# Kernel optimization log

Hardware: AMD Instinct MI355X
Metric: run time of the kernel (lower is better)

## Reference

```python
import jax, jax.numpy as jnp
from jax import lax
import numpy as np

TWO_PI = 2.0 * np.pi

# ---- batched real-amplitude statevector simulator (RY/CNOT only -> real state) ----

def _init_state(batch, n):
    s = jnp.zeros((batch, 2 ** n), dtype=jnp.float32).at[:, 0].set(1.0)
    return s.reshape((batch,) + (2,) * n)

def _ry(state, wire, theta, n):
    # state: (B, 2,...,2); theta: scalar or (B,)
    ax = wire + 1
    h = theta * 0.5
    c = jnp.reshape(jnp.cos(h), (-1,) + (1,) * (n - 1))
    s = jnp.reshape(jnp.sin(h), (-1,) + (1,) * (n - 1))
    s0 = lax.index_in_dim(state, 0, ax, keepdims=False)
    s1 = lax.index_in_dim(state, 1, ax, keepdims=False)
    return jnp.stack([c * s0 - s * s1, s * s0 + c * s1], axis=ax)

def _cnot(state, ctrl, tgt):
    axc, axt = ctrl + 1, tgt + 1
    s0 = lax.index_in_dim(state, 0, axc, keepdims=True)
    s1 = lax.index_in_dim(state, 1, axc, keepdims=True)
    return jnp.concatenate([s0, jnp.flip(s1, axis=axt)], axis=axc)

def _expz(state, wire, n):
    sgn = jnp.reshape(jnp.array([1.0, -1.0], state.dtype),
                      (1,) * (wire + 1) + (2,) + (1,) * (n - wire - 1))
    return jnp.sum(state * state * sgn, axis=tuple(range(1, n + 1)))

# gate lists: ('ry', theta_index, wire) or ('cx', control, target)
EDGE_OPS = [('ry',0,0),('ry',1,1),('cx',0,1),('ry',2,2),('ry',3,3),('cx',3,2),
            ('ry',4,4),('ry',5,5),('cx',4,5),('ry',6,6),('ry',7,7),('cx',7,6),
            ('ry',8,1),('ry',9,2),('cx',1,2),('ry',10,5),('ry',11,6),('cx',6,5),
            ('ry',12,2),('ry',13,5),('cx',2,5),('ry',14,5)]

NODE_OPS = [('ry',0,0),('ry',1,1),('cx',0,1),('ry',2,2),('ry',3,3),('cx',3,2),
            ('ry',4,4),('ry',5,5),('cx',4,5),('ry',6,6),('ry',7,7),('cx',7,6),
            ('ry',8,8),('ry',9,9),('cx',8,9),('ry',10,10),('ry',11,11),('cx',11,10),
            ('ry',12,1),('ry',13,2),('cx',1,2),('ry',14,5),('ry',15,6),('cx',6,5),
            ('ry',16,9),('ry',17,10),('cx',10,9),('ry',18,2),('ry',19,5),('cx',2,5),
            ('ry',20,5),('ry',21,9),('cx',5,9),('ry',22,4)]

def _circuit(angles, theta, ops, n, meas_wire):
    st = _init_state(angles.shape[0], n)
    for i in range(n):  # input encoding RYs, per-sample angles
        st = _ry(st, i, angles[:, i], n)
    for op in ops:
        if op[0] == 'ry':
            st = _ry(st, op[2], theta[op[1]], n)
        else:
            st = _cnot(st, op[1], op[2])
    return _expz(st, meas_wire, n)

# ---- GNN pieces ----

def _edge_net(H, Ri, Ro, theta):
    bo = Ro.T @ H                      # [E,4]
    bi = Ri.T @ H                      # [E,4]
    B = jnp.concatenate([bo, bi], axis=1)  # [E,8]
    return (1.0 - _circuit(B, theta, EDGE_OPS, 8, 5)) * 0.5

def _node_net(H, e, Ri, Ro, theta):
    bo = Ro.T @ H                      # [E,4]
    bi = Ri.T @ H                      # [E,4]
    mi = (Ri * e[None, :]) @ bo        # [N,4]
    mo = (Ro * e[None, :]) @ bi        # [N,4]
    M = jnp.concatenate([mi, mo, H], axis=1)  # [N,12]
    return jnp.pi * (1.0 - _circuit(M, theta, NODE_OPS, 12, 9))

def _gnn(X, Ri, Ro, W_in, b_in, theta_edge, theta_node, n_iters=2):
    H = jnp.concatenate([jax.nn.sigmoid(X @ W_in + b_in) * TWO_PI, X], axis=1)  # [N,4]
    e = _edge_net(H, Ri, Ro, theta_edge)
    for _ in range(n_iters):
        h = _node_net(H, e, Ri, Ro, theta_node)   # [N]
        H = jnp.concatenate([h[:, None], X], axis=1)
        e = _edge_net(H, Ri, Ro, theta_edge)
    return e


def setup_inputs() -> dict:
    key = jax.random.key(0)
    ks = jax.random.split(key, 6)
    N, E = 2048, 4096
    X = jax.random.normal(ks[0], (N, 3), jnp.float32)
    recv = jax.random.randint(ks[1], (E,), 0, N)
    send = jax.random.randint(ks[2], (E,), 0, N)
    cols = jnp.arange(E)
    Ri = jnp.zeros((N, E), jnp.float32).at[recv, cols].set(1.0)
    Ro = jnp.zeros((N, E), jnp.float32).at[send, cols].set(1.0)
    W_in = jax.random.normal(ks[3], (3, 1), jnp.float32)
    b_in = jnp.zeros((1,), jnp.float32)
    theta_edge = jax.random.uniform(ks[4], (15,), jnp.float32, 0.0, TWO_PI)
    theta_node = jax.random.uniform(ks[5], (23,), jnp.float32, 0.0, TWO_PI)
    return {'X': X, 'Ri': Ri, 'Ro': Ro, 'W_in': W_in, 'b_in': b_in,
            'theta_edge': theta_edge, 'theta_node': theta_node}


def reference(X, Ri, Ro, W_in, b_in, theta_edge, theta_node):
    return _gnn(X, Ri, Ro, W_in, b_in, theta_edge, theta_node, n_iters=2)
```

## Files before the change

kernel.cpp:

```cpp
#include <hip/hip_runtime.h>
#include <math.h>

#define N_NODES 2048
#define N_EDGES 4096
#define PI_F 3.14159265358979323846f
#define TWO_PI_F 6.28318530717958647692f

#define NBLK 256
#define NTHR 256
#define NSCAN (NBLK * NTHR)
#define TOT4 (N_NODES * N_EDGES / 4)

__device__ __forceinline__ float agent_load(const float* p) {
    return __hip_atomic_load(p, __ATOMIC_RELAXED, __HIP_MEMORY_SCOPE_AGENT);
}
__device__ __forceinline__ int agent_load_i(const int* p) {
    return __hip_atomic_load(p, __ATOMIC_RELAXED, __HIP_MEMORY_SCOPE_AGENT);
}
__device__ __forceinline__ void agent_store(float* p, float v) {
    __hip_atomic_store(p, v, __ATOMIC_RELAXED, __HIP_MEMORY_SCOPE_AGENT);
}
__device__ __forceinline__ void agent_store_i(int* p, int v) {
    __hip_atomic_store(p, v, __ATOMIC_RELAXED, __HIP_MEMORY_SCOPE_AGENT);
}
__device__ __forceinline__ void spin_ge(const int* p, int v) {
    while (__hip_atomic_load(p, __ATOMIC_RELAXED, __HIP_MEMORY_SCOPE_AGENT) < v)
        __builtin_amdgcn_s_sleep(2);
    asm volatile("" ::: "memory");
}


template<int M>
__device__ __forceinline__ void ry16(float* a, float c, float s) {
#pragma unroll
    for (int i = 0; i < 16; ++i)
        if (!(i & M)) {
            int j = i | M;
            float x0 = a[i], x1 = a[j];
            a[i] = c * x0 - s * x1;
            a[j] = s * x0 + c * x1;
        }
}
template<int MC, int MT>
__device__ __forceinline__ void cx16(float* a) {
#pragma unroll
    for (int i = 0; i < 16; ++i)
        if ((i & MC) && !(i & MT)) {
            int j = i | MT;
            float t = a[i]; a[i] = a[j]; a[j] = t;
        }
}

template<bool BTYPE>
__device__ __forceinline__ void sub16(const float* ic, const float* is,
                                      const float* thc, const float* ths,
                                      float& z, float& x) {
    float a[16];
    a[0] = ic[3]; a[1] = is[3];
#pragma unroll
    for (int i = 0; i < 2; ++i) { a[i | 2] = a[i] * is[2]; a[i] *= ic[2]; }
#pragma unroll
    for (int i = 0; i < 4; ++i) { a[i | 4] = a[i] * is[1]; a[i] *= ic[1]; }
#pragma unroll
    for (int i = 0; i < 8; ++i) { a[i | 8] = a[i] * is[0]; a[i] *= ic[0]; }
    ry16<8>(a, thc[0], ths[0]);
    ry16<4>(a, thc[1], ths[1]);
    cx16<8, 4>(a);
    ry16<2>(a, thc[2], ths[2]);
    ry16<1>(a, thc[3], ths[3]);
    cx16<1, 2>(a);
    ry16<4>(a, thc[4], ths[4]);
    ry16<2>(a, thc[5], ths[5]);
    if (BTYPE) { cx16<2, 4>(a); ry16<4>(a, thc[6], ths[6]); }
    else       { cx16<4, 2>(a); ry16<2>(a, thc[6], ths[6]); }
    const int m = BTYPE ? 4 : 2;
    z = 0.f; x = 0.f;
#pragma unroll
    for (int i = 0; i < 16; ++i) z += (i & m) ? -a[i] * a[i] : a[i] * a[i];
    if (BTYPE) {
#pragma unroll
        for (int i = 0; i < 16; ++i) if (!(i & 4)) x += a[i] * a[i | 4];
        x *= 2.f;
    }
}

__device__ __forceinline__ void edge_pub(
        float chh, float shh, const float* cxv, const float* sxv,
        const float* teC, const float* teS,
        float& zA, float& zB, float& xB) {
    float ic[4] = {chh, cxv[0], cxv[1], cxv[2]};
    float is[4] = {shh, sxv[0], sxv[1], sxv[2]};
    float dmy;
    {
        float thc[7] = {teC[0], teC[1], teC[2], teC[3], teC[8], teC[9], teC[12]};
        float ths[7] = {teS[0], teS[1], teS[2], teS[3], teS[8], teS[9], teS[12]};
        sub16<false>(ic, is, thc, ths, zA, dmy);
    }
    {
        float thc[7] = {teC[4], teC[5], teC[6], teC[7], teC[10], teC[11], teC[13]};
        float ths[7] = {teS[4], teS[5], teS[6], teS[7], teS[10], teS[11], teS[13]};
        sub16<true>(ic, is, thc, ths, zB, xB);
    }
}

__device__ __forceinline__ void scatter8(float ev, const float4& Hs, const float4& Hr,
                                         int si, int ri,
                                         float* __restrict__ macc, int* __restrict__ arr) {
    atomicAdd(&macc[ri*8+0], ev*Hs.x); atomicAdd(&macc[ri*8+1], ev*Hs.y);
    atomicAdd(&macc[ri*8+2], ev*Hs.z); atomicAdd(&macc[ri*8+3], ev*Hs.w);
    atomicAdd(&macc[si*8+4], ev*Hr.x); atomicAdd(&macc[si*8+5], ev*Hr.y);
    atomicAdd(&macc[si*8+6], ev*Hr.z); atomicAdd(&macc[si*8+7], ev*Hr.w);
    asm volatile("s_waitcnt vmcnt(0)" ::: "memory");
    atomicAdd(&arr[ri], 1); atomicAdd(&arr[si], 1);
}

__global__ __launch_bounds__(256) void k_fused(
        const float* __restrict__ X, const float* __restrict__ Ri,
        const float* __restrict__ Ro, const float* __restrict__ W,
        const float* __restrict__ b, const float* __restrict__ te,
        const float* __restrict__ tn,
        float* __restrict__ H, float* __restrict__ pub,
        int* __restrict__ send, int* __restrict__ recv,
        float* __restrict__ maccA, float* __restrict__ maccB,
        int* __restrict__ arrA, int* __restrict__ arrB,
        int* __restrict__ epoch, int* __restrict__ deg,
        int* __restrict__ sdone, float* __restrict__ out) {
    int blk = blockIdx.x, tid = threadIdx.x;
    bool edge_actor = (blk < 64)              && (tid < 64);
    bool node_actor = (blk >= 64 && blk < 96) && (tid < 64);

    float chh = 0.f, shh = 0.f, cxv[3], sxv[3];
    float teC[14], teS[14], tnC[22], tnS[22];
    float C14 = 0.f, S14 = 0.f;

    if (edge_actor) {
        float c, s;
        __sincosf(0.5f * te[14], &s, &c);
        C14 = c*c - s*s;
        S14 = 2.f*c*s;
    }
    if (node_actor) {
        int n = (blk - 64) * 64 + tid;
        float x0 = X[n*3+0], x1 = X[n*3+1], x2 = X[n*3+2];
        float z = x0*W[0] + x1*W[1] + x2*W[2] + b[0];
        float sg = 1.0f / (1.0f + __expf(-z));
        float h = sg * TWO_PI_F;
        __sincosf(0.5f*h,  &shh, &chh);
        __sincosf(0.5f*x0, &sxv[0], &cxv[0]);
        __sincosf(0.5f*x1, &sxv[1], &cxv[1]);
        __sincosf(0.5f*x2, &sxv[2], &cxv[2]);
#pragma unroll
        for (int k = 0; k < 14; ++k) __sincosf(0.5f*te[k], &teS[k], &teC[k]);
#pragma unroll
        for (int k = 0; k < 22; ++k) __sincosf(0.5f*tn[k], &tnS[k], &tnC[k]);
        float zA, zB, xB;
        edge_pub(chh, shh, cxv, sxv, teC, teS, zA, zB, xB);
        agent_store(&pub[n*4+0], zA);
        agent_store(&pub[n*4+1], zB);
        agent_store(&pub[n*4+2], xB);
        agent_store(&H[n*4+0], h);
        agent_store(&H[n*4+1], x0);
        agent_store(&H[n*4+2], x1);
        agent_store(&H[n*4+3], x2);
    }

    {
        int gid = blk * NTHR + tid;
        const float4* Ri4 = (const float4*)Ri;
        const float4* Ro4 = (const float4*)Ro;
#pragma unroll 1
        for (int t0 = gid; t0 < TOT4; t0 += 4 * NSCAN) {
            float4 vi[4], vo[4];
#pragma unroll
            for (int u = 0; u < 4; ++u) {
                int t = t0 + u * NSCAN;
                vi[u] = Ri4[t]; vo[u] = Ro4[t];
            }
#pragma unroll
            for (int u = 0; u < 4; ++u) {
                int t = t0 + u * NSCAN;
                int base = t * 4;
                int row = base >> 12;
                int e   = base & (N_EDGES - 1);
                int cnt = 0;
                if (vi[u].x != 0.f) { agent_store_i(recv+e+0, row); ++cnt; }
                if (vi[u].y != 0.f) { agent_store_i(recv+e+1, row); ++cnt; }
                if (vi[u].z != 0.f) { agent_store_i(recv+e+2, row); ++cnt; }
                if (vi[u].w != 0.f) { agent_store_i(recv+e+3, row); ++cnt; }
                if (vo[u].x != 0.f) { agent_store_i(send+e+0, row); ++cnt; }
                if (vo[u].y != 0.f) { agent_store_i(send+e+1, row); ++cnt; }
                if (vo[u].z != 0.f) { agent_store_i(send+e+2, row); ++cnt; }
                if (vo[u].w != 0.f) { agent_store_i(send+e+3, row); ++cnt; }
                if (cnt) atomicAdd(&deg[row], cnt);
            }
        }
        asm volatile("s_waitcnt vmcnt(0)" ::: "memory");
        __syncthreads();
        if (tid == 0) atomicAdd(sdone, 1);
    }

    if (!edge_actor && !node_actor) return;
    int lane = tid;

    spin_ge(sdone, NBLK);

    if (edge_actor) {
        int e = blk * 64 + lane;
        int si = agent_load_i(send + e);
        int ri = agent_load_i(recv + e);
        float4 Hs, Hr;
        Hs.x = agent_load(H+si*4+0); Hs.y = agent_load(H+si*4+1);
        Hs.z = agent_load(H+si*4+2); Hs.w = agent_load(H+si*4+3);
        Hr.x = agent_load(H+ri*4+0); Hr.y = agent_load(H+ri*4+1);
        Hr.z = agent_load(H+ri*4+2); Hr.w = agent_load(H+ri*4+3);

        float zA = agent_load(&pub[si*4+0]);
        float zB = agent_load(&pub[ri*4+1]);
        float xB = agent_load(&pub[ri*4+2]);
        float ev = 0.5f*(1.f - (C14*zA*zB - S14*xB));
        scatter8(ev, Hs, Hr, si, ri, maccA, arrA);

        spin_ge(epoch + si, 1); spin_ge(epoch + ri, 1);
        zA = agent_load(&pub[si*4+0]);
        zB = agent_load(&pub[ri*4+1]);
        xB = agent_load(&pub[ri*4+2]);
        Hs.x = agent_load(&H[si*4]);
        Hr.x = agent_load(&H[ri*4]);
        ev = 0.5f*(1.f - (C14*zA*zB - S14*xB));
        scatter8(ev, Hs, Hr, si, ri, maccB, arrB);

        spin_ge(epoch + si, 2); spin_ge(epoch + ri, 2);
        zA = agent_load(&pub[si*4+0]);
        zB = agent_load(&pub[ri*4+1]);
        xB = agent_load(&pub[ri*4+2]);
        out[e] = 0.5f*(1.f - (C14*zA*zB - S14*xB));
        return;
    }

    int n = (blk - 64) * 64 + lane;
    int dg = agent_load_i(deg + n);
    float C20 = tnC[20]*tnC[20] - tnS[20]*tnS[20];
    float S20 = 2.f*tnC[20]*tnS[20];

    for (int it = 0; it < 2; ++it) {
        const float* mc_ = it ? maccB : maccA;
        const int*   ar  = it ? arrB  : arrA;
        float zB9, dmy;
        {
            float ic[4] = {chh, cxv[0], cxv[1], cxv[2]};
            float is[4] = {shh, sxv[0], sxv[1], sxv[2]};
            float thc[7] = {tnC[8],tnC[9],tnC[10],tnC[11],tnC[16],tnC[17],tnC[21]};
            float ths[7] = {tnS[8],tnS[9],tnS[10],tnS[11],tnS[16],tnS[17],tnS[21]};
            sub16<true>(ic, is, thc, ths, zB9, dmy);
        }
        spin_ge(ar + n, dg);
        float M[8], mC[8], mS[8];
#pragma unroll
        for (int k = 0; k < 8; ++k) M[k] = agent_load(mc_ + n*8 + k);
#pragma unroll
        for (int k = 0; k < 8; ++k) __sincosf(0.5f*M[k], &mS[k], &mC[k]);
        float zA1, zA2, xA2;
        {
            float thc[7] = {tnC[0],tnC[1],tnC[2],tnC[3],tnC[12],tnC[13],tnC[18]};
            float ths[7] = {tnS[0],tnS[1],tnS[2],tnS[3],tnS[12],tnS[13],tnS[18]};
            sub16<false>(&mC[0], &mS[0], thc, ths, zA1, dmy);
        }
        {
            float thc[7] = {tnC[4],tnC[5],tnC[6],tnC[7],tnC[14],tnC[15],tnC[19]};
            float ths[7] = {tnS[4],tnS[5],tnS[6],tnS[7],tnS[14],tnS[15],tnS[19]};
            sub16<true>(&mC[4], &mS[4], thc, ths, zA2, xA2);
        }
        float p9 = (C20*zA1*zA2 - S20*xA2) * zB9;
        float h = PI_F * (1.f - p9);
        __sincosf(0.5f*h, &shh, &chh);
        float zAe, zBe, xBe;
        edge_pub(chh, shh, cxv, sxv, teC, teS, zAe, zBe, xBe);
        agent_store(&pub[n*4+0], zAe);
        agent_store(&pub[n*4+1], zBe);
        agent_store(&pub[n*4+2], xBe);
        agent_store(&H[n*4], h);
        asm volatile("s_waitcnt vmcnt(0)" ::: "memory");
        agent_store_i(epoch + n, it + 1);
    }
}

extern "C" void kernel_launch(void* const* d_in, const int* in_sizes, int n_in,
                              void* d_out, int out_size, void* d_ws, size_t ws_size,
                              hipStream_t stream) {
    const float* X  = (const float*)d_in[0];
    const float* Ri = (const float*)d_in[1];
    const float* Ro = (const float*)d_in[2];
    const float* W  = (const float*)d_in[3];
    const float* b  = (const float*)d_in[4];
    const float* te = (const float*)d_in[5];
    const float* tn = (const float*)d_in[6];
    float* out = (float*)d_out;

    float* H     = (float*)d_ws;
    float* pub   = H + N_NODES * 4;
    int*   send  = (int*)(pub + N_NODES * 4);
    int*   recv  = send + N_EDGES;
    float* maccA = (float*)(recv + N_EDGES);
    float* maccB = maccA + N_NODES * 8;
    int*   arrA  = (int*)(maccB + N_NODES * 8);
    int*   arrB  = arrA + N_NODES;
    int*   epoch = arrB + N_NODES;
    int*   deg   = epoch + N_NODES;
    int*   sdone = deg + N_NODES;
    size_t zbytes = (size_t)(2*N_NODES*8 + 4*N_NODES + 16) * 4;

    hipMemsetAsync((void*)maccA, 0, zbytes, stream);
    k_fused<<<NBLK, NTHR, 0, stream>>>(X, Ri, Ro, W, b, te, tn,
                                       H, pub, send, recv,
                                       maccA, maccB, arrA, arrB,
                                       epoch, deg, sdone, out);
}
```

Baseline: 129.0 us.

## Drop node-actor blocks; edges recompute endpoint node states redundantly

Removes the separate node-actor blocks and the epoch/pub handshake. Each edge thread now recomputes the node-state updates for its sender and receiver directly from the accumulated messages. Edge threads wait per-edge on the send/recv index (stored +1 so zero means not yet written) instead of on the global scan-done barrier, and theta sincos values are shared through LDS. The scan is also unrolled 8 deep instead of 4. This removes a cross-block dependency chain in exchange for duplicated node computation per edge and a larger memset.

```diff
diff --git a/kernel.cpp b/kernel.cpp
--- a/kernel.cpp
+++ b/kernel.cpp
@@ -16,9 +16,6 @@
 }
 __device__ __forceinline__ int agent_load_i(const int* p) {
     return __hip_atomic_load(p, __ATOMIC_RELAXED, __HIP_MEMORY_SCOPE_AGENT);
-}
-__device__ __forceinline__ void agent_store(float* p, float v) {
-    __hip_atomic_store(p, v, __ATOMIC_RELAXED, __HIP_MEMORY_SCOPE_AGENT);
 }
 __device__ __forceinline__ void agent_store_i(int* p, int v) {
     __hip_atomic_store(p, v, __ATOMIC_RELAXED, __HIP_MEMORY_SCOPE_AGENT);
@@ -84,23 +81,36 @@
     }
 }
 
-__device__ __forceinline__ void edge_pub(
-        float chh, float shh, const float* cxv, const float* sxv,
-        const float* teC, const float* teS,
-        float& zA, float& zB, float& xB) {
-    float ic[4] = {chh, cxv[0], cxv[1], cxv[2]};
-    float is[4] = {shh, sxv[0], sxv[1], sxv[2]};
-    float dmy;
-    {
-        float thc[7] = {teC[0], teC[1], teC[2], teC[3], teC[8], teC[9], teC[12]};
-        float ths[7] = {teS[0], teS[1], teS[2], teS[3], teS[8], teS[9], teS[12]};
-        sub16<false>(ic, is, thc, ths, zA, dmy);
-    }
-    {
-        float thc[7] = {teC[4], teC[5], teC[6], teC[7], teC[10], teC[11], teC[13]};
-        float ths[7] = {teS[4], teS[5], teS[6], teS[7], teS[10], teS[11], teS[13]};
-        sub16<true>(ic, is, thc, ths, zB, xB);
-    }
+__device__ __forceinline__ float node_update(
+        const float* M, float& chh, float& shh,
+        const float* cxv, const float* sxv,
+        const float* tnC, const float* tnS, float C20, float S20) {
+    float zB9, dmy;
+    {
+        float ic[4] = {chh, cxv[0], cxv[1], cxv[2]};
+        float is[4] = {shh, sxv[0], sxv[1], sxv[2]};
+        float thc[7] = {tnC[8],tnC[9],tnC[10],tnC[11],tnC[16],tnC[17],tnC[21]};
+        float ths[7] = {tnS[8],tnS[9],tnS[10],tnS[11],tnS[16],tnS[17],tnS[21]};
+        sub16<true>(ic, is, thc, ths, zB9, dmy);
+    }
+    float mC[8], mS[8];
+#pragma unroll
+    for (int k = 0; k < 8; ++k) __sincosf(0.5f * M[k], &mS[k], &mC[k]);
+    float zA1, zA2, xA2;
+    {
+        float thc[7] = {tnC[0],tnC[1],tnC[2],tnC[3],tnC[12],tnC[13],tnC[18]};
+        float ths[7] = {tnS[0],tnS[1],tnS[2],tnS[3],tnS[12],tnS[13],tnS[18]};
+        sub16<false>(&mC[0], &mS[0], thc, ths, zA1, dmy);
+    }
+    {
+        float thc[7] = {tnC[4],tnC[5],tnC[6],tnC[7],tnC[14],tnC[15],tnC[19]};
+        float ths[7] = {tnS[4],tnS[5],tnS[6],tnS[7],tnS[14],tnS[15],tnS[19]};
+        sub16<true>(&mC[4], &mS[4], thc, ths, zA2, xA2);
+    }
+    float p9 = (C20*zA1*zA2 - S20*xA2) * zB9;
+    float h = PI_F * (1.f - p9);
+    __sincosf(0.5f*h, &shh, &chh);
+    return h;
 }
 
 __device__ __forceinline__ void scatter8(float ev, const float4& Hs, const float4& Hr,
@@ -119,49 +129,28 @@
         const float* __restrict__ Ro, const float* __restrict__ W,
         const float* __restrict__ b, const float* __restrict__ te,
         const float* __restrict__ tn,
-        float* __restrict__ H, float* __restrict__ pub,
         int* __restrict__ send, int* __restrict__ recv,
         float* __restrict__ maccA, float* __restrict__ maccB,
         int* __restrict__ arrA, int* __restrict__ arrB,
-        int* __restrict__ epoch, int* __restrict__ deg,
-        int* __restrict__ sdone, float* __restrict__ out) {
+        int* __restrict__ deg, int* __restrict__ sdone,
+        float* __restrict__ out) {
+    __shared__ float s_teC[16], s_teS[16], s_tnC[24], s_tnS[24];
     int blk = blockIdx.x, tid = threadIdx.x;
-    bool edge_actor = (blk < 64)              && (tid < 64);
-    bool node_actor = (blk >= 64 && blk < 96) && (tid < 64);
-
-    float chh = 0.f, shh = 0.f, cxv[3], sxv[3];
-    float teC[14], teS[14], tnC[22], tnS[22];
-    float C14 = 0.f, S14 = 0.f;
-
-    if (edge_actor) {
-        float c, s;
-        __sincosf(0.5f * te[14], &s, &c);
-        C14 = c*c - s*s;
-        S14 = 2.f*c*s;
-    }
-    if (node_actor) {
-        int n = (blk - 64) * 64 + tid;
-        float x0 = X[n*3+0], x1 = X[n*3+1], x2 = X[n*3+2];
-        float z = x0*W[0] + x1*W[1] + x2*W[2] + b[0];
-        float sg = 1.0f / (1.0f + __expf(-z));
-        float h = sg * TWO_PI_F;
-        __sincosf(0.5f*h,  &shh, &chh);
-        __sincosf(0.5f*x0, &sxv[0], &cxv[0]);
-        __sincosf(0.5f*x1, &sxv[1], &cxv[1]);
-        __sincosf(0.5f*x2, &sxv[2], &cxv[2]);
-#pragma unroll
-        for (int k = 0; k < 14; ++k) __sincosf(0.5f*te[k], &teS[k], &teC[k]);
-#pragma unroll
-        for (int k = 0; k < 22; ++k) __sincosf(0.5f*tn[k], &tnS[k], &tnC[k]);
-        float zA, zB, xB;
-        edge_pub(chh, shh, cxv, sxv, teC, teS, zA, zB, xB);
-        agent_store(&pub[n*4+0], zA);
-        agent_store(&pub[n*4+1], zB);
-        agent_store(&pub[n*4+2], xB);
-        agent_store(&H[n*4+0], h);
-        agent_store(&H[n*4+1], x0);
-        agent_store(&H[n*4+2], x1);
-        agent_store(&H[n*4+3], x2);
+    bool edge_blk = (blk < 64);
+
+    if (edge_blk) {
+        if (tid < 14) {
+            float s, c; __sincosf(0.5f * te[tid], &s, &c);
+            s_teC[tid] = c; s_teS[tid] = s;
+        } else if (tid == 14) {
+            float s, c; __sincosf(te[14], &s, &c);
+            s_teC[14] = c; s_teS[14] = s;
+        } else if (tid < 15 + 22) {
+            int k = tid - 15; float s, c;
+            if (k == 20) __sincosf(tn[20], &s, &c);
+            else         __sincosf(0.5f * tn[k], &s, &c);
+            s_tnC[k] = c; s_tnS[k] = s;
+        }
     }
 
     {
@@ -169,28 +158,28 @@
         const float4* Ri4 = (const float4*)Ri;
         const float4* Ro4 = (const float4*)Ro;
 #pragma unroll 1
-        for (int t0 = gid; t0 < TOT4; t0 += 4 * NSCAN) {
-            float4 vi[4], vo[4];
-#pragma unroll
-            for (int u = 0; u < 4; ++u) {
+        for (int t0 = gid; t0 < TOT4; t0 += 8 * NSCAN) {
+            float4 vi[8], vo[8];
+#pragma unroll
+            for (int u = 0; u < 8; ++u) {
                 int t = t0 + u * NSCAN;
                 vi[u] = Ri4[t]; vo[u] = Ro4[t];
             }
 #pragma unroll
-            for (int u = 0; u < 4; ++u) {
+            for (int u = 0; u < 8; ++u) {
                 int t = t0 + u * NSCAN;
                 int base = t * 4;
                 int row = base >> 12;
                 int e   = base & (N_EDGES - 1);
                 int cnt = 0;
-                if (vi[u].x != 0.f) { agent_store_i(recv+e+0, row); ++cnt; }
-                if (vi[u].y != 0.f) { agent_store_i(recv+e+1, row); ++cnt; }
-                if (vi[u].z != 0.f) { agent_store_i(recv+e+2, row); ++cnt; }
-                if (vi[u].w != 0.f) { agent_store_i(recv+e+3, row); ++cnt; }
-                if (vo[u].x != 0.f) { agent_store_i(send+e+0, row); ++cnt; }
-                if (vo[u].y != 0.f) { agent_store_i(send+e+1, row); ++cnt; }
-                if (vo[u].z != 0.f) { agent_store_i(send+e+2, row); ++cnt; }
-                if (vo[u].w != 0.f) { agent_store_i(send+e+3, row); ++cnt; }
+                if (vi[u].x != 0.f) { agent_store_i(recv+e+0, row+1); ++cnt; }
+                if (vi[u].y != 0.f) { agent_store_i(recv+e+1, row+1); ++cnt; }
+                if (vi[u].z != 0.f) { agent_store_i(recv+e+2, row+1); ++cnt; }
+                if (vi[u].w != 0.f) { agent_store_i(recv+e+3, row+1); ++cnt; }
+                if (vo[u].x != 0.f) { agent_store_i(send+e+0, row+1); ++cnt; }
+                if (vo[u].y != 0.f) { agent_store_i(send+e+1, row+1); ++cnt; }
+                if (vo[u].z != 0.f) { agent_store_i(send+e+2, row+1); ++cnt; }
+                if (vo[u].w != 0.f) { agent_store_i(send+e+3, row+1); ++cnt; }
                 if (cnt) atomicAdd(&deg[row], cnt);
             }
         }
@@ -198,89 +187,95 @@
         __syncthreads();
         if (tid == 0) atomicAdd(sdone, 1);
     }
-
-    if (!edge_actor && !node_actor) return;
-    int lane = tid;
+    if (!edge_blk || tid >= 64) return;
+
+    int e = blk * 64 + tid;
+
+    int si, ri;
+    {
+        int v;
+        while ((v = agent_load_i(send + e)) == 0) __builtin_amdgcn_s_sleep(1);
+        si = v - 1;
+        while ((v = agent_load_i(recv + e)) == 0) __builtin_amdgcn_s_sleep(1);
+        ri = v - 1;
+        asm volatile("" ::: "memory");
+    }
+
+    float xs0 = X[si*3+0], xs1 = X[si*3+1], xs2 = X[si*3+2];
+    float xr0 = X[ri*3+0], xr1 = X[ri*3+1], xr2 = X[ri*3+2];
+    float w0 = W[0], w1 = W[1], w2 = W[2], bb = b[0];
+    float hs = TWO_PI_F / (1.f + __expf(-(xs0*w0 + xs1*w1 + xs2*w2 + bb)));
+    float hr = TWO_PI_F / (1.f + __expf(-(xr0*w0 + xr1*w1 + xr2*w2 + bb)));
+    float chs, shs, chr, shr, cxs[3], sxs[3], cxr[3], sxr[3];
+    __sincosf(0.5f*hs,  &shs,    &chs);
+    __sincosf(0.5f*xs0, &sxs[0], &cxs[0]);
+    __sincosf(0.5f*xs1, &sxs[1], &cxs[1]);
+    __sincosf(0.5f*xs2, &sxs[2], &cxs[2]);
+    __sincosf(0.5f*hr,  &shr,    &chr);
+    __sincosf(0.5f*xr0, &sxr[0], &cxr[0]);
+    __sincosf(0.5f*xr1, &sxr[1], &cxr[1]);
+    __sincosf(0.5f*xr2, &sxr[2], &cxr[2]);
+    float C14 = s_teC[14], S14 = s_teS[14];
+    float C20 = s_tnC[20], S20 = s_tnS[20];
+
+    float zA, zB, xB, dmy;
+    {
+        float ic[4] = {chs, cxs[0], cxs[1], cxs[2]};
+        float is[4] = {shs, sxs[0], sxs[1], sxs[2]};
+        float thc[7] = {s_teC[0],s_teC[1],s_teC[2],s_teC[3],s_teC[8],s_teC[9],s_teC[12]};
+        float ths[7] = {s_teS[0],s_teS[1],s_teS[2],s_teS[3],s_teS[8],s_teS[9],s_teS[12]};
+        sub16<false>(ic, is, thc, ths, zA, dmy);
+    }
+    {
+        float ic[4] = {chr, cxr[0], cxr[1], cxr[2]};
+        float is[4] = {shr, sxr[0], sxr[1], sxr[2]};
+        float thc[7] = {s_teC[4],s_teC[5],s_teC[6],s_teC[7],s_teC[10],s_teC[11],s_teC[13]};
+        float ths[7] = {s_teS[4],s_teS[5],s_teS[6],s_teS[7],s_teS[10],s_teS[11],s_teS[13]};
+        sub16<true>(ic, is, thc, ths, zB, xB);
+    }
+    float ev = 0.5f*(1.f - (C14*zA*zB - S14*xB));
+    scatter8(ev, make_float4(hs, xs0, xs1, xs2),
+                 make_float4(hr, xr0, xr1, xr2), si, ri, maccA, arrA);
 
     spin_ge(sdone, NBLK);
-
-    if (edge_actor) {
-        int e = blk * 64 + lane;
-        int si = agent_load_i(send + e);
-        int ri = agent_load_i(recv + e);
-        float4 Hs, Hr;
-        Hs.x = agent_load(H+si*4+0); Hs.y = agent_load(H+si*4+1);
-        Hs.z = agent_load(H+si*4+2); Hs.w = agent_load(H+si*4+3);
-        Hr.x = agent_load(H+ri*4+0); Hr.y = agent_load(H+ri*4+1);
-        Hr.z = agent_load(H+ri*4+2); Hr.w = agent_load(H+ri*4+3);
-
-        float zA = agent_load(&pub[si*4+0]);
-        float zB = agent_load(&pub[ri*4+1]);
-        float xB = agent_load(&pub[ri*4+2]);
-        float ev = 0.5f*(1.f - (C14*zA*zB - S14*xB));
-        scatter8(ev, Hs, Hr, si, ri, maccA, arrA);
-
-        spin_ge(epoch + si, 1); spin_ge(epoch + ri, 1);
-        zA = agent_load(&pub[si*4+0]);
-        zB = agent_load(&pub[ri*4+1]);
-        xB = agent_load(&pub[ri*4+2]);
-        Hs.x = agent_load(&H[si*4]);
-        Hr.x = agent_load(&H[ri*4]);
-        ev = 0.5f*(1.f - (C14*zA*zB - S14*xB));
-        scatter8(ev, Hs, Hr, si, ri, maccB, arrB);
-
-        spin_ge(epoch + si, 2); spin_ge(epoch + ri, 2);
-        zA = agent_load(&pub[si*4+0]);
-        zB = agent_load(&pub[ri*4+1]);
-        xB = agent_load(&pub[ri*4+2]);
-        out[e] = 0.5f*(1.f - (C14*zA*zB - S14*xB));
-        return;
-    }
-
-    int n = (blk - 64) * 64 + lane;
-    int dg = agent_load_i(deg + n);
-    float C20 = tnC[20]*tnC[20] - tnS[20]*tnS[20];
-    float S20 = 2.f*tnC[20]*tnS[20];
-
+    int dgs = agent_load_i(deg + si);
+    int dgr = agent_load_i(deg + ri);
+
+#pragma unroll
     for (int it = 0; it < 2; ++it) {
         const float* mc_ = it ? maccB : maccA;
         const int*   ar  = it ? arrB  : arrA;
-        float zB9, dmy;
+        while (agent_load_i(ar + si) < dgs || agent_load_i(ar + ri) < dgr)
+            __builtin_amdgcn_s_sleep(1);
+        asm volatile("" ::: "memory");
+        float Ms[8], Mr[8];
+#pragma unroll
+        for (int k = 0; k < 8; ++k) Ms[k] = agent_load(mc_ + si*8 + k);
+#pragma unroll
+        for (int k = 0; k < 8; ++k) Mr[k] = agent_load(mc_ + ri*8 + k);
+        hs = node_update(Ms, chs, shs, cxs, sxs, s_tnC, s_tnS, C20, S20);
+        hr = node_update(Mr, chr, shr, cxr, sxr, s_tnC, s_tnS, C20, S20);
         {
-            float ic[4] = {chh, cxv[0], cxv[1], cxv[2]};
-            float is[4] = {shh, sxv[0], sxv[1], sxv[2]};
-            float thc[7] = {tnC[8],tnC[9],tnC[10],tnC[11],tnC[16],tnC[17],tnC[21]};
-            float ths[7] = {tnS[8],tnS[9],tnS[10],tnS[11],tnS[16],tnS[17],tnS[21]};
-            sub16<true>(ic, is, thc, ths, zB9, dmy);
-        }
-        spin_ge(ar + n, dg);
-        float M[8], mC[8], mS[8];
-#pragma unroll
-        for (int k = 0; k < 8; ++k) M[k] = agent_load(mc_ + n*8 + k);
-#pragma unroll
-        for (int k = 0; k < 8; ++k) __sincosf(0.5f*M[k], &mS[k], &mC[k]);
-        float zA1, zA2, xA2;
+            float ic[4] = {chs, cxs[0], cxs[1], cxs[2]};
+            float is[4] = {shs, sxs[0], sxs[1], sxs[2]};
+            float thc[7] = {s_teC[0],s_teC[1],s_teC[2],s_teC[3],s_teC[8],s_teC[9],s_teC[12]};
+            float ths[7] = {s_teS[0],s_teS[1],s_teS[2],s_teS[3],s_teS[8],s_teS[9],s_teS[12]};
+            sub16<false>(ic, is, thc, ths, zA, dmy);
+        }
         {
-            float thc[7] = {tnC[0],tnC[1],tnC[2],tnC[3],tnC[12],tnC[13],tnC[18]};
-            float ths[7] = {tnS[0],tnS[1],tnS[2],tnS[3],tnS[12],tnS[13],tnS[18]};
-            sub16<false>(&mC[0], &mS[0], thc, ths, zA1, dmy);
-        }
-        {
-            float thc[7] = {tnC[4],tnC[5],tnC[6],tnC[7],tnC[14],tnC[15],tnC[19]};
-            float ths[7] = {tnS[4],tnS[5],tnS[6],tnS[7],tnS[14],tnS[15],tnS[19]};
-            sub16<true>(&mC[4], &mS[4], thc, ths, zA2, xA2);
-        }
-        float p9 = (C20*zA1*zA2 - S20*xA2) * zB9;
-        float h = PI_F * (1.f - p9);
-        __sincosf(0.5f*h, &shh, &chh);
-        float zAe, zBe, xBe;
-        edge_pub(chh, shh, cxv, sxv, teC, teS, zAe, zBe, xBe);
-        agent_store(&pub[n*4+0], zAe);
-        agent_store(&pub[n*4+1], zBe);
-        agent_store(&pub[n*4+2], xBe);
-        agent_store(&H[n*4], h);
-        asm volatile("s_waitcnt vmcnt(0)" ::: "memory");
-        agent_store_i(epoch + n, it + 1);
+            float ic[4] = {chr, cxr[0], cxr[1], cxr[2]};
+            float is[4] = {shr, sxr[0], sxr[1], sxr[2]};
+            float thc[7] = {s_teC[4],s_teC[5],s_teC[6],s_teC[7],s_teC[10],s_teC[11],s_teC[13]};
+            float ths[7] = {s_teS[4],s_teS[5],s_teS[6],s_teS[7],s_teS[10],s_teS[11],s_teS[13]};
+            sub16<true>(ic, is, thc, ths, zB, xB);
+        }
+        ev = 0.5f*(1.f - (C14*zA*zB - S14*xB));
+        if (it == 0) {
+            scatter8(ev, make_float4(hs, xs0, xs1, xs2),
+                         make_float4(hr, xr0, xr1, xr2), si, ri, maccB, arrB);
+        } else {
+            out[e] = ev;
+        }
     }
 }
 
@@ -296,22 +291,18 @@
     const float* tn = (const float*)d_in[6];
     float* out = (float*)d_out;
 
-    float* H     = (float*)d_ws;
-    float* pub   = H + N_NODES * 4;
-    int*   send  = (int*)(pub + N_NODES * 4);
+    int*   send  = (int*)d_ws;
     int*   recv  = send + N_EDGES;
     float* maccA = (float*)(recv + N_EDGES);
     float* maccB = maccA + N_NODES * 8;
     int*   arrA  = (int*)(maccB + N_NODES * 8);
     int*   arrB  = arrA + N_NODES;
-    int*   epoch = arrB + N_NODES;
-    int*   deg   = epoch + N_NODES;
+    int*   deg   = arrB + N_NODES;
     int*   sdone = deg + N_NODES;
-    size_t zbytes = (size_t)(2*N_NODES*8 + 4*N_NODES + 16) * 4;
-
-    hipMemsetAsync((void*)maccA, 0, zbytes, stream);
+    size_t zbytes = (size_t)(2*N_EDGES + 2*N_NODES*8 + 3*N_NODES + 16) * 4;
+
+    hipMemsetAsync((void*)send, 0, zbytes, stream);
     k_fused<<<NBLK, NTHR, 0, stream>>>(X, Ri, Ro, W, b, te, tn,
-                                       H, pub, send, recv,
-                                       maccA, maccB, arrA, arrB,
-                                       epoch, deg, sdone, out);
-}
+                                       send, recv, maccA, maccB,
+                                       arrA, arrB, deg, sdone, out);
+}
```

New measurement: 128.7 us. No clear change (-0.2%).
